# Kernel optimization log

Hardware: AMD Instinct MI355X
Metric: run time of the kernel (lower is better)

Reference implementation:

```python
import jax, jax.numpy as jnp
import numpy as np

N = 4096
C = 128
L = 4
E = 131072
HEADS = 4
BN_EPS = 1e-5


def setup_inputs() -> dict:
    key = jax.random.key(0)
    ks = jax.random.split(key, 16)
    s = jnp.float32(0.05)

    def rn(k, shape):
        return jax.random.normal(k, shape, dtype=jnp.float32) * s

    return {
        "x": jax.random.normal(ks[0], (N, C), dtype=jnp.float32),
        "edge_index": jax.random.randint(ks[1], (2, E), 0, N, dtype=jnp.int64) if jax.config.read("jax_enable_x64") else jax.random.randint(ks[1], (2, E), 0, N, dtype=jnp.int32),
        "gin_w1": rn(ks[2], (L, C, C)), "gin_b1": jnp.zeros((L, C), jnp.float32),
        "gin_w2": rn(ks[3], (L, C, C)), "gin_b2": jnp.zeros((L, C), jnp.float32),
        "attn_in_w": rn(ks[4], (L, 3 * C, C)), "attn_in_b": jnp.zeros((L, 3 * C), jnp.float32),
        "attn_out_w": rn(ks[5], (L, C, C)), "attn_out_b": jnp.zeros((L, C), jnp.float32),
        "n1_g": jnp.ones((L, C), jnp.float32), "n1_b": jnp.zeros((L, C), jnp.float32),
        "n2_g": jnp.ones((L, C), jnp.float32), "n2_b": jnp.zeros((L, C), jnp.float32),
        "n3_g": jnp.ones((L, C), jnp.float32), "n3_b": jnp.zeros((L, C), jnp.float32),
        "mlp_w1": rn(ks[6], (L, 2 * C, C)), "mlp_b1": jnp.zeros((L, 2 * C), jnp.float32),
        "mlp_w2": rn(ks[7], (L, C, 2 * C)), "mlp_b2": jnp.zeros((L, C), jnp.float32),
        "head_w1": rn(ks[8], (C // 2, C)), "head_b1": jnp.zeros((C // 2,), jnp.float32),
        "head_w2": rn(ks[9], (C // 4, C // 2)), "head_b2": jnp.zeros((C // 4,), jnp.float32),
        "head_w3": rn(ks[10], (1, C // 4)), "head_b3": jnp.zeros((1,), jnp.float32),
    }


def _bn(x, g, b):
    # BatchNorm1d over the node dim, training-mode (biased var), eps=1e-5
    mu = x.mean(axis=0)
    var = x.var(axis=0)
    return g * (x - mu) * jax.lax.rsqrt(var + BN_EPS) + b


def _gin(x, src, dst, w1, b1, w2, b2):
    # GINConv with eps=0: nn(x + sum_{j in N(i)} x_j)
    agg = jax.ops.segment_sum(x[src], dst, num_segments=x.shape[0])
    h = x + agg
    h = jnp.maximum(h @ w1.T + b1, 0.0)
    return h @ w2.T + b2


def _mha(x, wi, bi, wo, bo):
    # torch.nn.MultiheadAttention self-attention over a single dense batch of N nodes
    n, c = x.shape
    d = c // HEADS
    q, k, v = jnp.split(x @ wi.T + bi, 3, axis=-1)
    q = q.reshape(n, HEADS, d)
    k = k.reshape(n, HEADS, d)
    v = v.reshape(n, HEADS, d)
    scores = jnp.einsum('nhd,mhd->hnm', q, k) / jnp.sqrt(jnp.asarray(d, x.dtype))
    a = jax.nn.softmax(scores, axis=-1)
    o = jnp.einsum('hnm,mhd->nhd', a, v).reshape(n, c)
    return o @ wo.T + bo


def _forward(x, edge_index, gin_w1, gin_b1, gin_w2, gin_b2, attn_in_w, attn_in_b,
             attn_out_w, attn_out_b, n1_g, n1_b, n2_g, n2_b, n3_g, n3_b,
             mlp_w1, mlp_b1, mlp_w2, mlp_b2, head_w1, head_b1, head_w2, head_b2,
             head_w3, head_b3):
    src, dst = edge_index[0], edge_index[1]
    for i in range(L):
        # local GIN branch + residual + batch norm
        h1 = _bn(_gin(x, src, dst, gin_w1[i], gin_b1[i], gin_w2[i], gin_b2[i]) + x, n1_g[i], n1_b[i])
        # global attention branch + residual + batch norm
        h2 = _bn(_mha(x, attn_in_w[i], attn_in_b[i], attn_out_w[i], attn_out_b[i]) + x, n2_g[i], n2_b[i])
        h = h1 + h2
        # GPSConv MLP (C -> 2C -> C) with residual and final batch norm
        m = jnp.maximum(h @ mlp_w1[i].T + mlp_b1[i], 0.0) @ mlp_w2[i].T + mlp_b2[i]
        x = _bn(h + m, n3_g[i], n3_b[i])
    # head MLP: C -> C/2 -> C/4 -> 1
    h = jnp.maximum(x @ head_w1.T + head_b1, 0.0)
    h = jnp.maximum(h @ head_w2.T + head_b2, 0.0)
    return h @ head_w3.T + head_b3


def reference(x, edge_index, gin_w1, gin_b1, gin_w2, gin_b2, attn_in_w, attn_in_b,
              attn_out_w, attn_out_b, n1_g, n1_b, n2_g, n2_b, n3_g, n3_b,
              mlp_w1, mlp_b1, mlp_w2, mlp_b2, head_w1, head_b1, head_w2, head_b2,
              head_w3, head_b3):
    return _forward(x, edge_index, gin_w1, gin_b1, gin_w2, gin_b2, attn_in_w, attn_in_b,
                    attn_out_w, attn_out_b, n1_g, n1_b, n2_g, n2_b, n3_g, n3_b,
                    mlp_w1, mlp_b1, mlp_w2, mlp_b2, head_w1, head_b1, head_w2, head_b2,
                    head_w3, head_b3)
```

## Files before the change

### kernel.cpp

```cpp
#include <hip/hip_runtime.h>

#define N_NODES 4096
#define C_DIM   128
#define L_LAYERS 4
#define E_EDGES 131072
#define H_HEADS 4
#define D_HEAD  32
#define NC      (N_NODES * C_DIM)
#define NCu     (N_NODES * C_DIM)
#define P2S     40
#define HS_STRIDE 152
#define T2S       264
#define AT_S      136

typedef short bf16x8 __attribute__((ext_vector_type(8)));
typedef float f32x4  __attribute__((ext_vector_type(4)));

__device__ __forceinline__ unsigned short f2bf(float f) {
    unsigned int u = __float_as_uint(f);
    u += 0x7fffu + ((u >> 16) & 1u);
    return (unsigned short)(u >> 16);
}

__device__ __forceinline__ float bf_lo(unsigned int u) { return __uint_as_float(u << 16); }
__device__ __forceinline__ float bf_hi(unsigned int u) { return __uint_as_float(u & 0xffff0000u); }

__device__ __forceinline__ bf16x8 pack8(const float* v) {
    bf16x8 o;
#pragma unroll
    for (int i = 0; i < 8; ++i) o[i] = (short)f2bf(v[i]);
    return o;
}

__global__ __launch_bounds__(256) void hist_kernel(const int* __restrict__ ei,
                                                   int* __restrict__ deg) {
    int e = blockIdx.x * 256 + threadIdx.x;
    atomicAdd(&deg[ei[E_EDGES + e]], 1);
}

__global__ __launch_bounds__(256) void scan_kernel(const int* __restrict__ deg,
                                                   int* __restrict__ rowstart,
                                                   int* __restrict__ cursor) {
    __shared__ int ts[256];
    const int tid = threadIdx.x;
    int loc[16];
    int s = 0;
#pragma unroll
    for (int i = 0; i < 16; ++i) { loc[i] = s; s += deg[tid * 16 + i]; }
    ts[tid] = s;
    __syncthreads();
    for (int off = 1; off < 256; off <<= 1) {
        int t = (tid >= off) ? ts[tid - off] : 0;
        __syncthreads();
        if (tid >= off) ts[tid] += t;
        __syncthreads();
    }
    int off0 = ts[tid] - s;
#pragma unroll
    for (int i = 0; i < 16; ++i) {
        int v = off0 + loc[i];
        rowstart[tid * 16 + i] = v;
        cursor[tid * 16 + i] = v;
    }
    if (tid == 255) rowstart[4096] = off0 + s;
}

__global__ __launch_bounds__(256) void fill_kernel(const int* __restrict__ ei,
                                                   int* __restrict__ cursor,
                                                   int* __restrict__ csr_src) {
    int e = blockIdx.x * 256 + threadIdx.x;
    int d = ei[E_EDGES + e];
    int s = ei[e];
    int p = atomicAdd(&cursor[d], 1);
    csr_src[p] = s;
}

__global__ __launch_bounds__(256) void wcvt(const float* __restrict__ s0, const float* __restrict__ s1,
                                            const float* __restrict__ s2, const float* __restrict__ s3,
                                            const float* __restrict__ s4, const float* __restrict__ s5,
                                            unsigned short* __restrict__ wbf) {
    int i0 = (blockIdx.x * 256 + threadIdx.x) * 8;
    const float* src; int base;
    if      (i0 < 65536)  { src = s0; base = 0; }
    else if (i0 < 131072) { src = s1; base = 65536; }
    else if (i0 < 327680) { src = s2; base = 131072; }
    else if (i0 < 393216) { src = s3; base = 327680; }
    else if (i0 < 524288) { src = s4; base = 393216; }
    else                  { src = s5; base = 524288; }
    const float* p = src + (i0 - base);
    float t[8];
#pragma unroll
    for (int i = 0; i < 8; ++i) t[i] = p[i];
    *(bf16x8*)(wbf + i0) = pack8(t);
}

__global__ __launch_bounds__(256, 8) void qkv_gather(const float* __restrict__ xprev,
                                                     const float* __restrict__ st3,
                                                     const float* __restrict__ g3p,
                                                     const float* __restrict__ b3p,
                                                     const unsigned short* __restrict__ Wbf,
                                                     const float* __restrict__ bias,
                                                     unsigned short* __restrict__ Qb,
                                                     unsigned short* __restrict__ Kb,
                                                     unsigned short* __restrict__ VT,
                                                     const int* __restrict__ rowstart,
                                                     const int* __restrict__ csr_src,
                                                     float* __restrict__ ssz,
                                                     unsigned int* __restrict__ hsum) {
    __shared__ float scl2[2][128];
    __shared__ __align__(16) unsigned short at[16 * AT_S];

    const int b = blockIdx.x;
    const int tid = threadIdx.x;
    const float inv_n = 1.f / N_NODES;

    if (b < 1536) {
        const int ct = b % 6, rt = b / 6;
        const int rowbase = rt * 16;

        if (tid < 128) {
            float sc = 1.f, sh = 0.f;
            if (st3) {
                float m = st3[tid] * inv_n;
                float vv = st3[128 + tid] * inv_n - m * m;
                float r = rsqrtf(vv + 1e-5f);
                sc = g3p[tid] * r;
                sh = b3p[tid] - m * sc;
            }
            scl2[0][tid] = sc; scl2[1][tid] = sh;
        }
        __syncthreads();

        {
            const int e0 = tid * 8;
            const int r = e0 >> 7, c = e0 & 127;
            const float* xp = xprev + (size_t)(rowbase + r) * 128 + c;
            float t[8];
#pragma unroll
            for (int i = 0; i < 8; ++i) t[i] = xp[i] * scl2[0][c + i] + scl2[1][c + i];
            *(bf16x8*)(&at[r * AT_S + c]) = pack8(t);
        }
        __syncthreads();

        const int wv = tid >> 6;
        const int lane = tid & 63, lg = lane >> 4, ll = lane & 15;
        const int colbase = ct * 64 + wv * 16;
        const unsigned short* Wp = Wbf + (size_t)(colbase + ll) * 128 + lg * 8;

        f32x4 acc = {0.f, 0.f, 0.f, 0.f};
#pragma unroll
        for (int k = 0; k < 128; k += 32) {
            bf16x8 a = *(const bf16x8*)(&at[ll * AT_S + k + lg * 8]);
            bf16x8 w = *(const bf16x8*)(Wp + k);
            acc = __builtin_amdgcn_mfma_f32_16x16x32_bf16(a, w, acc, 0, 0, 0);
        }

        const float qsc = 0.25506973f;
        const int col = colbase + ll;
        const float bi = bias[col];
#pragma unroll
        for (int r = 0; r < 4; ++r) {
            const int row = rowbase + lg * 4 + r;
            float v = acc[r] + bi;
            if (col < 128) {
                int hh = col >> 5, d = col & 31;
                Qb[((size_t)hh * N_NODES + row) * D_HEAD + d] = f2bf(v * qsc);
            } else if (col < 256) {
                int c2 = col - 128, hh = c2 >> 5, d = c2 & 31;
                Kb[((size_t)hh * N_NODES + row) * D_HEAD + d] = f2bf(v);
            } else {
                int c2 = col - 256, hh = c2 >> 5, d = c2 & 31;
                VT[((size_t)hh * D_HEAD + d) * N_NODES + row] = f2bf(v);
            }
        }
    } else {
        if (b == 1536) {
            ssz[tid] = 0.f; ssz[256 + tid] = 0.f; ssz[512 + tid] = 0.f;
        }
        const int node = (b - 1536) * 4 + (tid >> 6);
        const int lane = tid & 63;
        const int ch0 = lane * 2, ch1 = ch0 + 1;
        float sc0 = 1.f, sh0 = 0.f, sc1 = 1.f, sh1 = 0.f;
        if (st3) {
            float m0 = st3[ch0] * inv_n;
            float v0 = st3[128 + ch0] * inv_n - m0 * m0;
            float r0 = rsqrtf(v0 + 1e-5f);
            sc0 = g3p[ch0] * r0; sh0 = b3p[ch0] - m0 * sc0;
            float m1 = st3[ch1] * inv_n;
            float v1 = st3[128 + ch1] * inv_n - m1 * m1;
            float r1 = rsqrtf(v1 + 1e-5f);
            sc1 = g3p[ch1] * r1; sh1 = b3p[ch1] - m1 * sc1;
        }
        const int beg = rowstart[node], end = rowstart[node + 1];
        float2 sv = *(const float2*)(xprev + (size_t)node * 128 + ch0);
        float ax = sv.x * sc0 + sh0, ay = sv.y * sc1 + sh1;
        float bx = 0.f, by = 0.f;
        int e = beg;
        for (; e + 4 <= end; e += 4) {
            int s0 = csr_src[e], s1 = csr_src[e + 1], s2 = csr_src[e + 2], s3 = csr_src[e + 3];
            float2 v0 = *(const float2*)(xprev + (size_t)s0 * 128 + ch0);
            float2 v1 = *(const float2*)(xprev + (size_t)s1 * 128 + ch0);
            float2 v2 = *(const float2*)(xprev + (size_t)s2 * 128 + ch0);
            float2 v3 = *(const float2*)(xprev + (size_t)s3 * 128 + ch0);
            ax += (v0.x * sc0 + sh0) + (v1.x * sc0 + sh0);
            ay += (v0.y * sc1 + sh1) + (v1.y * sc1 + sh1);
            bx += (v2.x * sc0 + sh0) + (v3.x * sc0 + sh0);
            by += (v2.y * sc1 + sh1) + (v3.y * sc1 + sh1);
        }
        for (; e < end; ++e) {
            float2 v0 = *(const float2*)(xprev + (size_t)csr_src[e] * 128 + ch0);
            ax += v0.x * sc0 + sh0; ay += v0.y * sc1 + sh1;
        }
        float ox = ax + bx, oy = ay + by;
        hsum[(size_t)node * 64 + lane] = (unsigned int)f2bf(ox) | ((unsigned int)f2bf(oy) << 16);
    }
}

__global__ __launch_bounds__(512, 4) void attn_gin1(const unsigned short* __restrict__ Qb,
                                                    const unsigned short* __restrict__ Kb,
                                                    const unsigned short* __restrict__ VT,
                                                    unsigned short* __restrict__ ob,
                                                    const unsigned short* __restrict__ hsum,
                                                    const unsigned short* __restrict__ W1,
                                                    const float* __restrict__ bias1,
                                                    unsigned short* __restrict__ t1out) {
    __shared__ __align__(16) float Ouns[8][16][33];
    __shared__ float Llp[8][16];

    const int b   = blockIdx.x;
    const int tid = threadIdx.x;
    const int wv  = tid >> 6;
    const int lane = tid & 63;
    const int lg  = lane >> 4;
    const int ll  = lane & 15;

    if (b >= 1024) {
        const int rowbase = (b - 1024) * 16;
        const int colbase = wv * 16;
        const unsigned short* Ap = hsum + (size_t)(rowbase + ll) * 128 + lg * 8;
        const unsigned short* Wp = W1 + (size_t)(colbase + ll) * 128 + lg * 8;
        f32x4 acc = {0.f, 0.f, 0.f, 0.f};
#pragma unroll
        for (int k = 0; k < 128; k += 32) {
            bf16x8 a = *(const bf16x8*)(Ap + k);
            bf16x8 w = *(const bf16x8*)(Wp + k);
            acc = __builtin_amdgcn_mfma_f32_16x16x32_bf16(a, w, acc, 0, 0, 0);
        }
        const int col = colbase + ll;
        const float bi = bias1[col];
#pragma unroll
        for (int r = 0; r < 4; ++r) {
            const int row = rowbase + lg * 4 + r;
            float v = fmaxf(acc[r] + bi, 0.f);
            t1out[(size_t)row * 128 + col] = f2bf(v);
        }
        return;
    }

    const int h   = b >> 8;
    const int q0  = (b & 255) * 16;

    const unsigned short* Qh = Qb + ((size_t)h * N_NODES + q0) * D_HEAD;
    const unsigned short* Kh = Kb + (size_t)h * N_NODES * D_HEAD;
    const unsigned short* Vh = VT + (size_t)h * D_HEAD * N_NODES;

    bf16x8 qf0 = *(const bf16x8*)(Qh + ll * D_HEAD + lg * 8);

    f32x4 o00 = {0.f,0.f,0.f,0.f}, o01 = {0.f,0.f,0.f,0.f};
    float l0[4] = {0.f,0.f,0.f,0.f};

    unsigned short* Pw = (unsigned short*)(void*)Ouns + wv * (16 * P2S);
    const int k0 = wv * (N_NODES / 8);
    const unsigned short* Vrow_lo = Vh + (size_t)ll * N_NODES;
    const unsigned short* Vrow_hi = Vh + (size_t)(16 + ll) * N_NODES;

    for (int t = 0; t < (N_NODES / 8) / 128; ++t) {
        const int kt = k0 + t * 128;
#pragma unroll
        for (int j = 0; j < 4; ++j) {
#pragma unroll
            for (int w = 0; w < 2; ++w) {
                const int kc = 2 * j + w;
                bf16x8 kf = *(const bf16x8*)(Kh + (size_t)(kt + kc * 16 + ll) * D_HEAD + lg * 8);
                f32x4 z = {0.f, 0.f, 0.f, 0.f};
                f32x4 d0 = __builtin_amdgcn_mfma_f32_16x16x32_bf16(qf0, kf, z, 0, 0, 0);
#pragma unroll
                for (int r = 0; r < 4; ++r) {
                    float p0 = exp2f(d0[r]); l0[r] += p0;
                    Pw[(lg * 4 + r) * P2S + w * 16 + ll] = f2bf(p0);
                }
            }
            asm volatile("" ::: "memory");

            const int kb = kt + 32 * j + lg * 8;
            bf16x8 va = *(const bf16x8*)(Vrow_lo + kb);
            bf16x8 vb = *(const bf16x8*)(Vrow_hi + kb);
            bf16x8 pf0 = *(const bf16x8*)(Pw + ll * P2S + lg * 8);
            o00 = __builtin_amdgcn_mfma_f32_16x16x32_bf16(pf0, va, o00, 0, 0, 0);
            o01 = __builtin_amdgcn_mfma_f32_16x16x32_bf16(pf0, vb, o01, 0, 0, 0);
            asm volatile("" ::: "memory");
        }
    }

#pragma unroll
    for (int r = 0; r < 4; ++r) {
#pragma unroll
        for (int off = 1; off < 16; off <<= 1)
            l0[r] += __shfl_xor(l0[r], off, 64);
    }

    __syncthreads();

#pragma unroll
    for (int r = 0; r < 4; ++r) {
        Ouns[wv][lg * 4 + r][ll]      = o00[r];
        Ouns[wv][lg * 4 + r][16 + ll] = o01[r];
    }
    if (ll == 0) {
#pragma unroll
        for (int r = 0; r < 4; ++r)
            Llp[wv][lg * 4 + r] = l0[r];
    }
    __syncthreads();

    {
        const int row = tid >> 5, col = tid & 31;
        float L = 0.f, oa = 0.f;
#pragma unroll
        for (int w = 0; w < 8; ++w) {
            L  += Llp[w][row];
            oa += Ouns[w][row][col];
        }
        ob[(size_t)(q0 + row) * C_DIM + h * D_HEAD + col] = f2bf(oa / L);
    }
}

__global__ __launch_bounds__(256, 8) void gemm2x(const unsigned short* __restrict__ A0,
                                                 const unsigned short* __restrict__ W0,
                                                 const float* __restrict__ bias0,
                                                 float* __restrict__ out0,
                                                 float* __restrict__ stats0,
                                                 const unsigned short* __restrict__ A1,
                                                 const unsigned short* __restrict__ W1,
                                                 const float* __restrict__ bias1,
                                                 float* __restrict__ out1,
                                                 float* __restrict__ stats1,
                                                 const float* __restrict__ xprev,
                                                 const float* __restrict__ st3,
                                                 const float* __restrict__ g3p,
                                                 const float* __restrict__ b3p) {
    const int b = blockIdx.x;
    const int which = b >> 9;
    const int bl = b & 511;
    const unsigned short* Abf = which ? A1 : A0;
    const unsigned short* Wbf = which ? W1 : W0;
    const float* bias = which ? bias1 : bias0;
    float* outf  = which ? out1 : out0;
    float* stats = which ? stats1 : stats0;

    const int tid = threadIdx.x;
    const int wv = tid >> 6;
    const int lane = tid & 63, lg = lane >> 4, ll = lane & 15;
    const int rowbase = (bl >> 1) * 16;
    const int colbase = (bl & 1) * 64 + wv * 16;

    const unsigned short* Ap = Abf + (size_t)(rowbase + ll) * 128 + lg * 8;
    const unsigned short* Wp = Wbf + (size_t)(colbase + ll) * 128 + lg * 8;

    f32x4 acc = {0.f, 0.f, 0.f, 0.f};
#pragma unroll
    for (int k = 0; k < 128; k += 32) {
        bf16x8 a = *(const bf16x8*)(Ap + k);
        bf16x8 w = *(const bf16x8*)(Wp + k);
        acc = __builtin_amdgcn_mfma_f32_16x16x32_bf16(a, w, acc, 0, 0, 0);
    }

    const int col = colbase + ll;
    const float bi = bias[col];
    float sc = 1.f, sh = 0.f;
    if (st3) {
        const float inv_n = 1.f / N_NODES;
        float m = st3[col] * inv_n;
        float vv = st3[128 + col] * inv_n - m * m;
        float r = rsqrtf(vv + 1e-5f);
        sc = g3p[col] * r; sh = b3p[col] - m * sc;
    }
    float sv = 0.f, sv2 = 0.f;
#pragma unroll
    for (int r = 0; r < 4; ++r) {
        const int row = rowbase + lg * 4 + r;
        float v = acc[r] + bi + (xprev[(size_t)row * 128 + col] * sc + sh);
        outf[(size_t)row * 128 + col] = v;
        sv += v; sv2 += v * v;
    }
    sv  += __shfl_xor(sv, 16, 64);  sv  += __shfl_xor(sv, 32, 64);
    sv2 += __shfl_xor(sv2, 16, 64); sv2 += __shfl_xor(sv2, 32, 64);
    if (lg == 0) {
        atomicAdd(&stats[col], sv);
        atomicAdd(&stats[128 + col], sv2);
    }
}

__global__ __launch_bounds__(256) void mlp_fused(const float* __restrict__ g1p,
                                                 const float* __restrict__ a2p,
                                                 const float* __restrict__ st1,
                                                 const float* __restrict__ st2,
                                                 const float* __restrict__ g1v,
                                                 const float* __restrict__ b1v,
                                                 const float* __restrict__ g2v,
                                                 const float* __restrict__ b2v,
                                                 const unsigned short* __restrict__ W1bf,
                                                 const float* __restrict__ bias1,
                                                 const unsigned short* __restrict__ W2bf,
                                                 const float* __restrict__ bias2,
                                                 float* __restrict__ m3out,
                                                 float* __restrict__ stats3) {
    __shared__ float hf[16][132];
    __shared__ __align__(16) unsigned short hs[16 * HS_STRIDE];
    __shared__ __align__(16) unsigned short t2s[16 * T2S];
    __shared__ float scl[4][128];

    const int tid = threadIdx.x;
    const int rowbase = blockIdx.x * 16;
    const float inv_n = 1.f / N_NODES;

    if (tid < 128) {
        const int ch = tid;
        float m1 = st1[ch] * inv_n;
        float v1 = st1[128 + ch] * inv_n - m1 * m1;
        float r1 = rsqrtf(v1 + 1e-5f);
        float sc1 = g1v[ch] * r1;
        scl[0][ch] = sc1;
        scl[1][ch] = b1v[ch] - m1 * sc1;
        float m2 = st2[ch] * inv_n;
        float v2 = st2[128 + ch] * inv_n - m2 * m2;
        float r2 = rsqrtf(v2 + 1e-5f);
        float sc2 = g2v[ch] * r2;
        scl[2][ch] = sc2;
        scl[3][ch] = b2v[ch] - m2 * sc2;
    }
    __syncthreads();

#pragma unroll
    for (int j = tid; j < 512; j += 256) {
        const int r = j >> 5, cq = (j & 31) * 4;
        float4 v1 = *(const float4*)(g1p + (size_t)(rowbase + r) * 128 + cq);
        float4 v2 = *(const float4*)(a2p + (size_t)(rowbase + r) * 128 + cq);
        float h0 = v1.x * scl[0][cq]     + scl[1][cq]     + v2.x * scl[2][cq]     + scl[3][cq];
        float h1 = v1.y * scl[0][cq + 1] + scl[1][cq + 1] + v2.y * scl[2][cq + 1] + scl[3][cq + 1];
        float h2 = v1.z * scl[0][cq + 2] + scl[1][cq + 2] + v2.z * scl[2][cq + 2] + scl[3][cq + 2];
        float h3 = v1.w * scl[0][cq + 3] + scl[1][cq + 3] + v2.w * scl[2][cq + 3] + scl[3][cq + 3];
        hf[r][cq] = h0; hf[r][cq + 1] = h1; hf[r][cq + 2] = h2; hf[r][cq + 3] = h3;
        ushort4 u;
        u.x = f2bf(h0); u.y = f2bf(h1); u.z = f2bf(h2); u.w = f2bf(h3);
        *(ushort4*)(&hs[r * HS_STRIDE + cq]) = u;
    }
    __syncthreads();

    const int wv = tid >> 6;
    const int lane = tid & 63, lg = lane >> 4, ll = lane & 15;

#pragma unroll
    for (int ct = 0; ct < 4; ++ct) {
        const int colbase = wv * 16 + ct * 64;
        const unsigned short* Wp = W1bf + (size_t)(colbase + ll) * 128 + lg * 8;
        f32x4 acc = {0.f, 0.f, 0.f, 0.f};
#pragma unroll
        for (int k = 0; k < 128; k += 32) {
            bf16x8 a = *(const bf16x8*)(&hs[ll * HS_STRIDE + k + lg * 8]);
            bf16x8 w = *(const bf16x8*)(Wp + k);
            acc = __builtin_amdgcn_mfma_f32_16x16x32_bf16(a, w, acc, 0, 0, 0);
        }
        const int col = colbase + ll;
        const float bi = bias1[col];
#pragma unroll
        for (int r = 0; r < 4; ++r) {
            float v = fmaxf(acc[r] + bi, 0.f);
            t2s[(lg * 4 + r) * T2S + col] = f2bf(v);
        }
    }
    __syncthreads();

#pragma unroll
    for (int p = 0; p < 2; ++p) {
        const int colbase = p * 64 + wv * 16;
        const unsigned short* Wp = W2bf + (size_t)(colbase + ll) * 256 + lg * 8;
        f32x4 acc = {0.f, 0.f, 0.f, 0.f};
#pragma unroll
        for (int k = 0; k < 256; k += 32) {
            bf16x8 a = *(const bf16x8*)(&t2s[ll * T2S + k + lg * 8]);
            bf16x8 w = *(const bf16x8*)(Wp + k);
            acc = __builtin_amdgcn_mfma_f32_16x16x32_bf16(a, w, acc, 0, 0, 0);
        }
        const int col = colbase + ll;
        const float bi = bias2[col];
        float sv = 0.f, sv2 = 0.f;
#pragma unroll
        for (int r = 0; r < 4; ++r) {
            const int row = lg * 4 + r;
            float v = acc[r] + bi + hf[row][col];
            m3out[(size_t)(rowbase + row) * 128 + col] = v;
            sv += v; sv2 += v * v;
        }
        sv  += __shfl_xor(sv, 16, 64);  sv  += __shfl_xor(sv, 32, 64);
        sv2 += __shfl_xor(sv2, 16, 64); sv2 += __shfl_xor(sv2, 32, 64);
        if (lg == 0) {
            atomicAdd(&stats3[col], sv);
            atomicAdd(&stats3[128 + col], sv2);
        }
    }
}

__global__ __launch_bounds__(256) void head_fused(const float* __restrict__ m3p,
                                                  const float* __restrict__ st3,
                                                  const float* __restrict__ g3p,
                                                  const float* __restrict__ b3p,
                                                  const float* __restrict__ w1,
                                                  const float* __restrict__ b1,
                                                  const float* __restrict__ w2,
                                                  const float* __restrict__ b2,
                                                  const float* __restrict__ w3,
                                                  const float* __restrict__ b3,
                                                  float* __restrict__ out) {
    __shared__ __align__(16) float xs[8][128];
    __shared__ __align__(16) float hs2[8][64];
    __shared__ float scl2[2][128];
    const int tid = threadIdx.x;
    const int n = tid >> 5;
    const int g = tid & 31;
    const int node0 = blockIdx.x * 8;
    const float inv_n = 1.f / N_NODES;

    if (tid < 128) {
        float m = st3[tid] * inv_n;
        float vv = st3[128 + tid] * inv_n - m * m;
        float r = rsqrtf(vv + 1e-5f);
        float sc = g3p[tid] * r;
        scl2[0][tid] = sc;
        scl2[1][tid] = b3p[tid] - m * sc;
    }
    __syncthreads();

    {
        const int e0 = tid * 4;
        const int r = e0 >> 7, c = e0 & 127;
        float4 v = *(const float4*)(m3p + (size_t)(node0 + r) * 128 + c);
        xs[r][c]     = v.x * scl2[0][c]     + scl2[1][c];
        xs[r][c + 1] = v.y * scl2[0][c + 1] + scl2[1][c + 1];
        xs[r][c + 2] = v.z * scl2[0][c + 2] + scl2[1][c + 2];
        xs[r][c + 3] = v.w * scl2[0][c + 3] + scl2[1][c + 3];
    }
    __syncthreads();

    {
        float acc0 = b1[g], acc1 = b1[g + 32];
        const float* wa = w1 + (size_t)g * 128;
        const float* wb = w1 + (size_t)(g + 32) * 128;
#pragma unroll 8
        for (int k = 0; k < 128; k += 4) {
            float4 xv = *(const float4*)(&xs[n][k]);
            float4 va = *(const float4*)(wa + k);
            float4 vb = *(const float4*)(wb + k);
            acc0 += xv.x * va.x + xv.y * va.y + xv.z * va.z + xv.w * va.w;
            acc1 += xv.x * vb.x + xv.y * vb.y + xv.z * vb.z + xv.w * vb.w;
        }
        hs2[n][g]      = fmaxf(acc0, 0.f);
        hs2[n][g + 32] = fmaxf(acc1, 0.f);
    }
    __syncthreads();

    {
        float acc = b2[g];
        const float* wr = w2 + (size_t)g * 64;
#pragma unroll 8
        for (int k = 0; k < 64; k += 4) {
            float4 hv = *(const float4*)(&hs2[n][k]);
            float4 wv = *(const float4*)(wr + k);
            acc += hv.x * wv.x + hv.y * wv.y + hv.z * wv.z + hv.w * wv.w;
        }
        float t = fmaxf(acc, 0.f) * w3[g];
#pragma unroll
        for (int off = 1; off < 32; off <<= 1) t += __shfl_xor(t, off, 64);
        if (g == 0) out[node0 + n] = t + b3[0];
    }
}

extern "C" void kernel_launch(void* const* d_in, const int* in_sizes, int n_in,
                              void* d_out, int out_size, void* d_ws, size_t ws_size,
                              hipStream_t stream) {
    (void)in_sizes; (void)n_in; (void)out_size; (void)ws_size;
    const float* x_in   = (const float*)d_in[0];
    const int*   ei     = (const int*)d_in[1];
    const float* gin_w1 = (const float*)d_in[2];
    const float* gin_b1 = (const float*)d_in[3];
    const float* gin_w2 = (const float*)d_in[4];
    const float* gin_b2 = (const float*)d_in[5];
    const float* ain_w  = (const float*)d_in[6];
    const float* ain_b  = (const float*)d_in[7];
    const float* aout_w = (const float*)d_in[8];
    const float* aout_b = (const float*)d_in[9];
    const float* n1_g   = (const float*)d_in[10];
    const float* n1_b   = (const float*)d_in[11];
    const float* n2_g   = (const float*)d_in[12];
    const float* n2_b   = (const float*)d_in[13];
    const float* n3_g   = (const float*)d_in[14];
    const float* n3_b   = (const float*)d_in[15];
    const float* mlp_w1 = (const float*)d_in[16];
    const float* mlp_b1 = (const float*)d_in[17];
    const float* mlp_w2 = (const float*)d_in[18];
    const float* mlp_b2 = (const float*)d_in[19];
    const float* h_w1   = (const float*)d_in[20];
    const float* h_b1   = (const float*)d_in[21];
    const float* h_w2   = (const float*)d_in[22];
    const float* h_b2   = (const float*)d_in[23];
    const float* h_w3   = (const float*)d_in[24];
    const float* h_b3   = (const float*)d_in[25];

    float* f = (float*)d_ws;
    float* g1   = f;
    float* a2   = f + 1 * (size_t)NC;
    float* t1ch = f + 2 * (size_t)NC;
    float* m3   = f + 3 * (size_t)NC;
    unsigned short* R1  = (unsigned short*)(f + 4 * (size_t)NC);
    unsigned short* Qb      = R1;
    unsigned short* Kb      = R1 + (size_t)NCu;
    unsigned short* VT      = R1 + 2 * (size_t)NCu;
    unsigned short* R2      = R1 + 3 * (size_t)NCu;
    unsigned short* ao_bf   = R2;
    unsigned short* hsum_bf = (unsigned short*)a2;
    unsigned short* t1_bf   = (unsigned short*)t1ch;
    unsigned short* wbf     = R2 + (size_t)NCu;
    float* ssA    = (float*)(wbf + 655360);
    float* ssB    = ssA + 768;
    int* ibase    = (int*)(ssB + 768);
    int* deg      = ibase;
    int* rowstart = ibase + 4096;
    int* cursor   = ibase + 4096 + 4098;
    int* csr_src  = ibase + 4096 + 4098 + 4096;

    const int OG1 = 0, OG2 = 65536, OAI = 131072, OAO = 327680, OM1 = 393216, OM2 = 524288;

    hipMemsetAsync(deg, 0, 4096 * sizeof(int), stream);
    hist_kernel<<<E_EDGES / 256, 256, 0, stream>>>(ei, deg);
    scan_kernel<<<1, 256, 0, stream>>>(deg, rowstart, cursor);
    fill_kernel<<<E_EDGES / 256, 256, 0, stream>>>(ei, cursor, csr_src);
    wcvt<<<320, 256, 0, stream>>>(gin_w1, gin_w2, ain_w, aout_w, mlp_w1, mlp_w2, wbf);

    for (int i = 0; i < L_LAYERS; ++i) {
        const float* xprev = (i == 0) ? x_in : m3;
        const float* st3p  = (i == 0) ? nullptr : ((i & 1) ? ssA : ssB) + 512;
        const float* g3p   = (i == 0) ? nullptr : n3_g + (size_t)(i - 1) * C_DIM;
        const float* b3p   = (i == 0) ? nullptr : n3_b + (size_t)(i - 1) * C_DIM;
        float* ss_cur = (i & 1) ? ssB : ssA;
        const float* gb1 = gin_b1 + (size_t)i * C_DIM;
        const float* gb2 = gin_b2 + (size_t)i * C_DIM;
        const float* aib = ain_b + (size_t)i * 3 * C_DIM;
        const float* aob = aout_b + (size_t)i * C_DIM;
        const float* mb1 = mlp_b1 + (size_t)i * 2 * C_DIM;
        const float* mb2 = mlp_b2 + (size_t)i * C_DIM;

        qkv_gather<<<2560, 256, 0, stream>>>(xprev, st3p, g3p, b3p,
                                             wbf + OAI + (size_t)i * 49152, aib,
                                             Qb, Kb, VT, rowstart, csr_src,
                                             ss_cur, (unsigned int*)hsum_bf);
        attn_gin1<<<1280, 512, 0, stream>>>(Qb, Kb, VT, ao_bf,
                                            hsum_bf, wbf + OG1 + (size_t)i * 16384, gb1, t1_bf);
        gemm2x<<<1024, 256, 0, stream>>>(t1_bf, wbf + OG2 + (size_t)i * 16384, gb2, g1, ss_cur,
                                         ao_bf, wbf + OAO + (size_t)i * 16384, aob, a2, ss_cur + 256,
                                         xprev, st3p, g3p, b3p);
        mlp_fused<<<256, 256, 0, stream>>>(g1, a2, ss_cur, ss_cur + 256,
                                           n1_g + (size_t)i * C_DIM, n1_b + (size_t)i * C_DIM,
                                           n2_g + (size_t)i * C_DIM, n2_b + (size_t)i * C_DIM,
                                           wbf + OM1 + (size_t)i * 32768, mb1,
                                           wbf + OM2 + (size_t)i * 32768, mb2,
                                           m3, ss_cur + 512);
    }

    head_fused<<<N_NODES / 8, 256, 0, stream>>>(m3, ssB + 512,
                                                n3_g + 3 * (size_t)C_DIM, n3_b + 3 * (size_t)C_DIM,
                                                h_w1, h_b1, h_w2, h_b2, h_w3, h_b3,
                                                (float*)d_out);
}
```

Measured before the change: 424.8 us.

## Process 64 queries per attention block to reuse K/V loads

Each attention block now handles 64 query rows per head (four 16-row fragments) instead of 16, so every K and V fragment loaded from global memory feeds four MFMAs rather than one. The grid shrinks from 1024 to 256 attention blocks, and the shared-memory staging for P, partial outputs and row sums grows fourfold. The occupancy hint drops to 2 blocks per CU, and s_setprio raises wave priority around the MFMA/exp section. The cost is more registers per thread and fewer waves in flight to hide latency, with only 256 attention blocks plus 256 GIN blocks in the grid.

```diff
diff --git a/kernel.cpp b/kernel.cpp
--- a/kernel.cpp
+++ b/kernel.cpp
@@ -216,7 +216,7 @@
     }
 }
 
-__global__ __launch_bounds__(512, 4) void attn_gin1(const unsigned short* __restrict__ Qb,
+__global__ __launch_bounds__(512, 2) void attn_gin1(const unsigned short* __restrict__ Qb,
                                                     const unsigned short* __restrict__ Kb,
                                                     const unsigned short* __restrict__ VT,
                                                     unsigned short* __restrict__ ob,
@@ -224,8 +224,8 @@
                                                     const unsigned short* __restrict__ W1,
                                                     const float* __restrict__ bias1,
                                                     unsigned short* __restrict__ t1out) {
-    __shared__ __align__(16) float Ouns[8][16][33];
-    __shared__ float Llp[8][16];
+    __shared__ __align__(16) float Ouns[8][64][33];
+    __shared__ float Llp[8][64];
 
     const int b   = blockIdx.x;
     const int tid = threadIdx.x;
@@ -234,8 +234,8 @@
     const int lg  = lane >> 4;
     const int ll  = lane & 15;
 
-    if (b >= 1024) {
-        const int rowbase = (b - 1024) * 16;
+    if (b >= 256) {
+        const int rowbase = (b - 256) * 16;
         const int colbase = wv * 16;
         const unsigned short* Ap = hsum + (size_t)(rowbase + ll) * 128 + lg * 8;
         const unsigned short* Wp = W1 + (size_t)(colbase + ll) * 128 + lg * 8;
@@ -257,19 +257,31 @@
         return;
     }
 
-    const int h   = b >> 8;
-    const int q0  = (b & 255) * 16;
+    const int h   = b >> 6;
+    const int q0  = (b & 63) * 64;
 
     const unsigned short* Qh = Qb + ((size_t)h * N_NODES + q0) * D_HEAD;
     const unsigned short* Kh = Kb + (size_t)h * N_NODES * D_HEAD;
     const unsigned short* Vh = VT + (size_t)h * D_HEAD * N_NODES;
 
-    bf16x8 qf0 = *(const bf16x8*)(Qh + ll * D_HEAD + lg * 8);
-
-    f32x4 o00 = {0.f,0.f,0.f,0.f}, o01 = {0.f,0.f,0.f,0.f};
-    float l0[4] = {0.f,0.f,0.f,0.f};
-
-    unsigned short* Pw = (unsigned short*)(void*)Ouns + wv * (16 * P2S);
+    bf16x8 qf[4];
+#pragma unroll
+    for (int fq = 0; fq < 4; ++fq)
+        qf[fq] = *(const bf16x8*)(Qh + (fq * 16 + ll) * D_HEAD + lg * 8);
+
+    f32x4 oacc[4][2];
+#pragma unroll
+    for (int fq = 0; fq < 4; ++fq) {
+        oacc[fq][0] = (f32x4){0.f, 0.f, 0.f, 0.f};
+        oacc[fq][1] = (f32x4){0.f, 0.f, 0.f, 0.f};
+    }
+    float lsum[4][4];
+#pragma unroll
+    for (int fq = 0; fq < 4; ++fq)
+#pragma unroll
+        for (int r = 0; r < 4; ++r) lsum[fq][r] = 0.f;
+
+    unsigned short* Pw = (unsigned short*)(void*)Ouns + wv * (64 * P2S);
     const int k0 = wv * (N_NODES / 8);
     const unsigned short* Vrow_lo = Vh + (size_t)ll * N_NODES;
     const unsigned short* Vrow_hi = Vh + (size_t)(16 + ll) * N_NODES;
@@ -278,16 +290,21 @@
         const int kt = k0 + t * 128;
 #pragma unroll
         for (int j = 0; j < 4; ++j) {
+            __builtin_amdgcn_s_setprio(1);
 #pragma unroll
             for (int w = 0; w < 2; ++w) {
                 const int kc = 2 * j + w;
                 bf16x8 kf = *(const bf16x8*)(Kh + (size_t)(kt + kc * 16 + ll) * D_HEAD + lg * 8);
-                f32x4 z = {0.f, 0.f, 0.f, 0.f};
-                f32x4 d0 = __builtin_amdgcn_mfma_f32_16x16x32_bf16(qf0, kf, z, 0, 0, 0);
-#pragma unroll
-                for (int r = 0; r < 4; ++r) {
-                    float p0 = exp2f(d0[r]); l0[r] += p0;
-                    Pw[(lg * 4 + r) * P2S + w * 16 + ll] = f2bf(p0);
+#pragma unroll
+                for (int fq = 0; fq < 4; ++fq) {
+                    f32x4 z = {0.f, 0.f, 0.f, 0.f};
+                    f32x4 d = __builtin_amdgcn_mfma_f32_16x16x32_bf16(qf[fq], kf, z, 0, 0, 0);
+#pragma unroll
+                    for (int r = 0; r < 4; ++r) {
+                        float p = exp2f(d[r]);
+                        lsum[fq][r] += p;
+                        Pw[(fq * 16 + lg * 4 + r) * P2S + w * 16 + ll] = f2bf(p);
+                    }
                 }
             }
             asm volatile("" ::: "memory");
@@ -295,43 +312,57 @@
             const int kb = kt + 32 * j + lg * 8;
             bf16x8 va = *(const bf16x8*)(Vrow_lo + kb);
             bf16x8 vb = *(const bf16x8*)(Vrow_hi + kb);
-            bf16x8 pf0 = *(const bf16x8*)(Pw + ll * P2S + lg * 8);
-            o00 = __builtin_amdgcn_mfma_f32_16x16x32_bf16(pf0, va, o00, 0, 0, 0);
-            o01 = __builtin_amdgcn_mfma_f32_16x16x32_bf16(pf0, vb, o01, 0, 0, 0);
+#pragma unroll
+            for (int fq = 0; fq < 4; ++fq) {
+                bf16x8 pf = *(const bf16x8*)(Pw + (fq * 16 + ll) * P2S + lg * 8);
+                oacc[fq][0] = __builtin_amdgcn_mfma_f32_16x16x32_bf16(pf, va, oacc[fq][0], 0, 0, 0);
+                oacc[fq][1] = __builtin_amdgcn_mfma_f32_16x16x32_bf16(pf, vb, oacc[fq][1], 0, 0, 0);
+            }
+            __builtin_amdgcn_s_setprio(0);
             asm volatile("" ::: "memory");
         }
     }
 
 #pragma unroll
-    for (int r = 0; r < 4; ++r) {
-#pragma unroll
-        for (int off = 1; off < 16; off <<= 1)
-            l0[r] += __shfl_xor(l0[r], off, 64);
-    }
-
-    __syncthreads();
-
-#pragma unroll
-    for (int r = 0; r < 4; ++r) {
-        Ouns[wv][lg * 4 + r][ll]      = o00[r];
-        Ouns[wv][lg * 4 + r][16 + ll] = o01[r];
-    }
+    for (int fq = 0; fq < 4; ++fq)
+#pragma unroll
+        for (int r = 0; r < 4; ++r) {
+#pragma unroll
+            for (int off = 1; off < 16; off <<= 1)
+                lsum[fq][r] += __shfl_xor(lsum[fq][r], off, 64);
+        }
+
+    __syncthreads();
+
+#pragma unroll
+    for (int fq = 0; fq < 4; ++fq)
+#pragma unroll
+        for (int r = 0; r < 4; ++r) {
+            Ouns[wv][fq * 16 + lg * 4 + r][ll]      = oacc[fq][0][r];
+            Ouns[wv][fq * 16 + lg * 4 + r][16 + ll] = oacc[fq][1][r];
+        }
     if (ll == 0) {
 #pragma unroll
-        for (int r = 0; r < 4; ++r)
-            Llp[wv][lg * 4 + r] = l0[r];
+        for (int fq = 0; fq < 4; ++fq)
+#pragma unroll
+            for (int r = 0; r < 4; ++r)
+                Llp[wv][fq * 16 + lg * 4 + r] = lsum[fq][r];
     }
     __syncthreads();
 
     {
-        const int row = tid >> 5, col = tid & 31;
-        float L = 0.f, oa = 0.f;
-#pragma unroll
-        for (int w = 0; w < 8; ++w) {
-            L  += Llp[w][row];
-            oa += Ouns[w][row][col];
-        }
-        ob[(size_t)(q0 + row) * C_DIM + h * D_HEAD + col] = f2bf(oa / L);
+        const int row = tid >> 3, c0 = (tid & 7) * 4;
+        float L = 0.f;
+#pragma unroll
+        for (int w = 0; w < 8; ++w) L += Llp[w][row];
+        const float inv = 1.f / L;
+#pragma unroll
+        for (int c = 0; c < 4; ++c) {
+            float oa = 0.f;
+#pragma unroll
+            for (int w = 0; w < 8; ++w) oa += Ouns[w][row][c0 + c];
+            ob[(size_t)(q0 + row) * C_DIM + h * D_HEAD + c0 + c] = f2bf(oa * inv);
+        }
     }
 }
 
@@ -663,8 +694,8 @@
                                              wbf + OAI + (size_t)i * 49152, aib,
                                              Qb, Kb, VT, rowstart, csr_src,
                                              ss_cur, (unsigned int*)hsum_bf);
-        attn_gin1<<<1280, 512, 0, stream>>>(Qb, Kb, VT, ao_bf,
-                                            hsum_bf, wbf + OG1 + (size_t)i * 16384, gb1, t1_bf);
+        attn_gin1<<<512, 512, 0, stream>>>(Qb, Kb, VT, ao_bf,
+                                           hsum_bf, wbf + OG1 + (size_t)i * 16384, gb1, t1_bf);
         gemm2x<<<1024, 256, 0, stream>>>(t1_bf, wbf + OG2 + (size_t)i * 16384, gb2, g1, ss_cur,
                                          ao_bf, wbf + OAO + (size_t)i * 16384, aob, a2, ss_cur + 256,
                                          xprev, st3p, g3p, b3p);
```

After: 363.5 us. 1.17x faster.
